# Kernel optimization log

Measured on AMD Instinct MI355X. Metric: run time of the kernel, lower is better.

The kernel has to match this reference:

```python
import jax, jax.numpy as jnp
import numpy as np

DECAY = 0.99
EPS = 1e-05


def setup_inputs() -> dict:
    key = jax.random.key(0)
    k1, k2, k3, k4 = jax.random.split(key, 4)
    B, T, D, K = 16, 4096, 128, 1024
    return {
        "z": jax.random.normal(k1, (B, T, D), dtype=jnp.float32),
        "embedding": jax.random.normal(k2, (K, D), dtype=jnp.float32),
        "cluster_size": jax.random.uniform(k3, (K,), dtype=jnp.float32),
        "ema_w": jax.random.normal(k4, (K, D), dtype=jnp.float32),
    }


def reference(z, embedding, cluster_size, ema_w):
    B, T, D = z.shape
    K = embedding.shape[0]
    z_flat = z.reshape(B * T, D)

    # Squared-distance matrix [N, K]: ||z||^2 - 2 z E^T + ||E||^2
    dist = (
        jnp.sum(z_flat * z_flat, axis=1, keepdims=True)
        - 2.0 * (z_flat @ embedding.T)
        + jnp.sum(embedding * embedding, axis=1)
    )
    indices = jnp.argmin(dist, axis=1)  # [N]
    z_q = embedding[indices].reshape(B, T, D)

    # EMA codebook update (training branch); segment_sum == one_hot.T @ z, one_hot.sum(0)
    batch_cluster = jax.ops.segment_sum(
        jnp.ones((B * T,), dtype=z.dtype), indices, num_segments=K
    )
    new_cluster_size = cluster_size * DECAY + (1.0 - DECAY) * batch_cluster
    batch_ema = jax.ops.segment_sum(z_flat, indices, num_segments=K)
    new_ema_w = ema_w * DECAY + (1.0 - DECAY) * batch_ema

    n = jnp.sum(new_cluster_size)
    smoothed = (new_cluster_size + EPS) / (n + K * EPS) * n
    new_embedding = new_ema_w / smoothed[:, None]

    # Commitment loss on OLD codebook vectors (matches torch order of ops)
    loss_vq = jnp.mean(jnp.square(jax.lax.stop_gradient(z_q) - z))
    # Straight-through estimator
    z_q_st = z + jax.lax.stop_gradient(z_q - z)

    return (
        z_q_st,
        indices.reshape(B, T),
        loss_vq,
        new_embedding,
        new_cluster_size,
        new_ema_w,
    )
```

## Files before the change

kernel.cpp:

```cpp
#include <hip/hip_runtime.h>

#define K_CODES 1024
#define D_DIM 128
#define N_ROWS 65536
#define DECAY_F 0.99f
#define OMD_F 0.01f
#define EPS_F 1e-5f

#define EPAD 144
#define CHUNK_CODES 64
#define N_CHUNKS 16
#define CHUNK_USHORT (2 * CHUNK_CODES * EPAD)
#define NT 2
#define SEG_TILE 64

#define WS_CNT     0
#define WS_LOSS    1024
#define WS_BE      1028
#define WS_ZERO_END (1028 + 131072)
#define WS_ENORM   132100
#define WS_SMOOTH  133124
#define WS_CUR     134148
#define WS_FIDX    135172
#define WS_BUCKET  200708
#define WS_SCODE   266244
#define WS_EIMG    331780

typedef __bf16 bf8_t __attribute__((ext_vector_type(8)));
typedef float  f4_t  __attribute__((ext_vector_type(4)));

__device__ inline unsigned short f2bf_bits(float f) {
    __bf16 h = (__bf16)f;
    return __builtin_bit_cast(unsigned short, h);
}
__device__ inline float bf_bits2f(unsigned short u) {
    __bf16 h = __builtin_bit_cast(__bf16, u);
    return (float)h;
}

__device__ inline void gld16(const void* g, void* l) {
    __builtin_amdgcn_global_load_lds(
        (const __attribute__((address_space(1))) void*)g,
        (__attribute__((address_space(3))) void*)l, 16, 0, 0);
}

__global__ void vq_prep(const float* __restrict__ emb, float* __restrict__ enorm,
                        unsigned short* __restrict__ eimg) {
    int t = blockIdx.x * blockDim.x + threadIdx.x;
    int code = t >> 5;
    int q = t & 31;
    float4 v = ((const float4*)(emb + (size_t)code * D_DIM))[q];
    int chunk = code >> 6, c = code & 63;
    size_t hbase = (size_t)chunk * CHUNK_USHORT + (size_t)c * EPAD + q * 4;
    size_t lbase = hbase + (size_t)CHUNK_CODES * EPAD;
    float vv[4] = {v.x, v.y, v.z, v.w};
    ushort4 hi, lo;
    unsigned short* hp = (unsigned short*)&hi;
    unsigned short* lp = (unsigned short*)&lo;
#pragma unroll
    for (int i = 0; i < 4; ++i) {
        unsigned short hb = f2bf_bits(vv[i]);
        hp[i] = hb;
        lp[i] = f2bf_bits(vv[i] - bf_bits2f(hb));
    }
    *(ushort4*)(eimg + hbase) = hi;
    *(ushort4*)(eimg + lbase) = lo;

    float s = v.x * v.x + v.y * v.y + v.z * v.z + v.w * v.w;
#pragma unroll
    for (int o = 1; o < 32; o <<= 1) s += __shfl_xor(s, o, 64);
    if (q == 0) enorm[code] = s;
}

__device__ inline void top2_update(float s, int code, float& s1, int& i1, float& s2, int& i2) {
    bool b1 = s < s1;
    bool b2 = s < s2;
    s2 = b1 ? s1 : (b2 ? s : s2);
    i2 = b1 ? i1 : (b2 ? code : i2);
    s1 = b1 ? s : s1;
    i1 = b1 ? code : i1;
}

__device__ inline void top2_merge(float& s1, int& i1, float& s2, int& i2,
                                  float t1, int j1, float t2, int j2) {
    bool bf = (t1 < s1) || (t1 == s1 && j1 < i1);
    float ns1 = bf ? t1 : s1;  int ni1 = bf ? j1 : i1;
    float ca  = bf ? s1 : t1;  int ia  = bf ? i1 : j1;
    float cb  = bf ? t2 : s2;  int ib  = bf ? j2 : i2;
    bool bs = (ca < cb) || (ca == cb && ia < ib);
    s1 = ns1; i1 = ni1;
    s2 = bs ? ca : cb; i2 = bs ? ia : ib;
}

__global__ __launch_bounds__(512) void vq_score(
    const float* __restrict__ z, const unsigned short* __restrict__ eimg,
    const float* __restrict__ enorm_g, const float* __restrict__ emb,
    float* __restrict__ out_zq, float* __restrict__ out_idx,
    int* __restrict__ cnt, unsigned int* __restrict__ fidx,
    float* __restrict__ loss_acc)
{
    __shared__ __align__(16) unsigned short lds[2][CHUNK_USHORT];
    __shared__ __align__(16) float lds_en[K_CODES];

    const int tid  = threadIdx.x;
    const int wv   = tid >> 6;
    const int lane = tid & 63;
    const int l16  = lane & 15;
    const int quad = lane >> 4;
    const int rowbase = blockIdx.x * 256 + wv * 32;

    if (tid < 256) ((float4*)lds_en)[tid] = ((const float4*)enorm_g)[tid];

    {
        const char* gs = (const char*)eimg;
        char* ls = (char*)&lds[0][0];
#pragma unroll
        for (int i = 0; i < 5; ++i) {
            int idx = wv * 5 + i;
            if (idx < 36) gld16(gs + idx * 1024 + lane * 16, ls + idx * 1024);
        }
    }

    bf8_t zh[NT][4], zl[NT][4];
#pragma unroll
    for (int nt = 0; nt < NT; ++nt) {
        int row = rowbase + nt * 16 + l16;
        const float* zr = z + (size_t)row * D_DIM;
#pragma unroll
        for (int ks = 0; ks < 4; ++ks) {
            const float4* p = (const float4*)(zr + ks * 32 + quad * 8);
            float4 a = p[0], b = p[1];
            float v[8] = {a.x, a.y, a.z, a.w, b.x, b.y, b.z, b.w};
#pragma unroll
            for (int i = 0; i < 8; ++i) {
                __bf16 hh = (__bf16)v[i];
                zh[nt][ks][i] = hh;
                zl[nt][ks][i] = (__bf16)(v[i] - (float)hh);
            }
        }
    }

    float s1[NT], s2[NT];
    int   i1[NT], i2[NT];
#pragma unroll
    for (int nt = 0; nt < NT; ++nt) { s1[nt] = 3.4e38f; s2[nt] = 3.4e38f; i1[nt] = 0; i2[nt] = 0; }

    __syncthreads();

    for (int c = 0; c < N_CHUNKS; ++c) {
        const int cur = c & 1;
        if (c + 1 < N_CHUNKS) {
            const char* gs = (const char*)(eimg + (size_t)(c + 1) * CHUNK_USHORT);
            char* ls = (char*)&lds[1 - cur][0];
#pragma unroll
            for (int i = 0; i < 5; ++i) {
                int idx = wv * 5 + i;
                if (idx < 36) gld16(gs + idx * 1024 + lane * 16, ls + idx * 1024);
            }
        }
        const unsigned short* buf = &lds[cur][0];

#pragma unroll
        for (int cg = 0; cg < 2; ++cg) {
            f4_t acc[2][NT];
#pragma unroll
            for (int ct = 0; ct < 2; ++ct)
#pragma unroll
                for (int nt = 0; nt < NT; ++nt) acc[ct][nt] = (f4_t)(0.f);

#pragma unroll
            for (int ks = 0; ks < 4; ++ks) {
                bf8_t ah[2], al[2];
#pragma unroll
                for (int ct = 0; ct < 2; ++ct) {
                    int cl = cg * 32 + ct * 16 + l16;
                    int base = cl * EPAD + ks * 32 + quad * 8;
                    ah[ct] = *(const bf8_t*)&buf[base];
                    al[ct] = *(const bf8_t*)&buf[CHUNK_CODES * EPAD + base];
                }
#pragma unroll
                for (int ct = 0; ct < 2; ++ct)
#pragma unroll
                    for (int nt = 0; nt < NT; ++nt) {
                        acc[ct][nt] = __builtin_amdgcn_mfma_f32_16x16x32_bf16(
                            ah[ct], zh[nt][ks], acc[ct][nt], 0, 0, 0);
                        acc[ct][nt] = __builtin_amdgcn_mfma_f32_16x16x32_bf16(
                            al[ct], zh[nt][ks], acc[ct][nt], 0, 0, 0);
                        acc[ct][nt] = __builtin_amdgcn_mfma_f32_16x16x32_bf16(
                            ah[ct], zl[nt][ks], acc[ct][nt], 0, 0, 0);
                    }
            }

#pragma unroll
            for (int ct = 0; ct < 2; ++ct) {
                int cb = c * 64 + cg * 32 + ct * 16 + quad * 4;
                float4 en4 = *(const float4*)&lds_en[cb];
                float env[4] = {en4.x, en4.y, en4.z, en4.w};
#pragma unroll
                for (int nt = 0; nt < NT; ++nt)
#pragma unroll
                    for (int r = 0; r < 4; ++r) {
                        float s = env[r] - 2.0f * acc[ct][nt][r];
                        top2_update(s, cb + r, s1[nt], i1[nt], s2[nt], i2[nt]);
                    }
            }
        }
        __syncthreads();
    }

#pragma unroll
    for (int off = 16; off <= 32; off <<= 1) {
#pragma unroll
        for (int nt = 0; nt < NT; ++nt) {
            float t1 = __shfl_xor(s1[nt], off, 64);
            int   j1 = __shfl_xor(i1[nt], off, 64);
            float t2 = __shfl_xor(s2[nt], off, 64);
            int   j2 = __shfl_xor(i2[nt], off, 64);
            top2_merge(s1[nt], i1[nt], s2[nt], i2[nt], t1, j1, t2, j2);
        }
    }

    float ls = 0.f;
#pragma unroll
    for (int nt = 0; nt < NT; ++nt) {
        int row = rowbase + nt * 16 + l16;
        int j1 = i1[nt], j2 = i2[nt];

        const float4* zp  = (const float4*)(z   + (size_t)row * D_DIM);
        const float4* e1p = (const float4*)(emb + (size_t)j1  * D_DIM);
        const float4* e2p = (const float4*)(emb + (size_t)j2  * D_DIM);

        float4 zv[8], a1[8], a2[8];
#pragma unroll
        for (int ks = 0; ks < 4; ++ks) {
            int o = ks * 8 + quad * 2;
            zv[ks * 2]     = zp[o];   zv[ks * 2 + 1] = zp[o + 1];
            a1[ks * 2]     = e1p[o];  a1[ks * 2 + 1] = e1p[o + 1];
            a2[ks * 2]     = e2p[o];  a2[ks * 2 + 1] = e2p[o + 1];
        }
        float p1 = 0.f, p2 = 0.f;
#pragma unroll
        for (int i = 0; i < 8; ++i) {
            p1 += zv[i].x * a1[i].x + zv[i].y * a1[i].y + zv[i].z * a1[i].z + zv[i].w * a1[i].w;
            p2 += zv[i].x * a2[i].x + zv[i].y * a2[i].y + zv[i].z * a2[i].z + zv[i].w * a2[i].w;
        }
        p1 += __shfl_xor(p1, 16, 64); p1 += __shfl_xor(p1, 32, 64);
        p2 += __shfl_xor(p2, 16, 64); p2 += __shfl_xor(p2, 32, 64);
        float sc1 = lds_en[j1] - 2.0f * p1;
        float sc2 = lds_en[j2] - 2.0f * p2;
        bool use2 = (sc2 < sc1) || (sc2 == sc1 && j2 < j1);
        int best = use2 ? j2 : j1;

        if (quad == 0) {
            out_idx[row] = (float)best;
            fidx[row] = (unsigned int)best;
            atomicAdd(cnt + best, 1);
        }

        float4* oz = (float4*)(out_zq + (size_t)row * D_DIM);
#pragma unroll
        for (int i = 0; i < 8; ++i) {
            float4 q = use2 ? a2[i] : a1[i];
            float4 zvv = zv[i];
            float4 df = {q.x - zvv.x, q.y - zvv.y, q.z - zvv.z, q.w - zvv.w};
            ls += df.x * df.x + df.y * df.y + df.z * df.z + df.w * df.w;
            float4 o = {zvv.x + df.x, zvv.y + df.y, zvv.z + df.z, zvv.w + df.w};
            oz[(i >> 1) * 8 + quad * 2 + (i & 1)] = o;
        }
    }

#pragma unroll
    for (int off = 32; off > 0; off >>= 1) ls += __shfl_down(ls, off, 64);
    if (lane == 0) atomicAdd(loss_acc, ls);
}

__global__ void vq_scan(const int* __restrict__ cnt, int* __restrict__ cursor)
{
    __shared__ int tmp[K_CODES];
    int k = threadIdx.x;
    int c = cnt[k];
    tmp[k] = c;
    __syncthreads();
    for (int off = 1; off < K_CODES; off <<= 1) {
        int t = (k >= off) ? tmp[k - off] : 0;
        __syncthreads();
        tmp[k] += t;
        __syncthreads();
    }
    cursor[k] = tmp[k] - c;
}

__global__ void vq_scatter(const unsigned int* __restrict__ fidx,
                           int* __restrict__ cursor, unsigned int* __restrict__ bucket,
                           int* __restrict__ scode)
{
    int row = blockIdx.x * blockDim.x + threadIdx.x;
    int k = (int)fidx[row];
    int slot = atomicAdd(cursor + k, 1);
    bucket[slot] = (unsigned int)row;
    scode[slot]  = k;
}

__global__ __launch_bounds__(128) void vq_segsum(
    const float* __restrict__ z, const unsigned int* __restrict__ bucket,
    const int* __restrict__ scode, float* __restrict__ be)
{
    __shared__ int sb[SEG_TILE];
    __shared__ int sc[SEG_TILE];
    const int tid = threadIdx.x;
    const int t0  = blockIdx.x * SEG_TILE;

    if (tid < SEG_TILE) sb[tid] = (int)bucket[t0 + tid];
    else if (tid < 2 * SEG_TILE) sc[tid - SEG_TILE] = scode[t0 + tid - SEG_TILE];
    __syncthreads();

    const int d = tid;
    float acc = 0.f;
    int cur = sc[0];

    for (int i = 0; i < SEG_TILE; i += 8) {
        float v[8];
#pragma unroll
        for (int j = 0; j < 8; ++j)
            v[j] = z[(size_t)sb[i + j] * D_DIM + d];
#pragma unroll
        for (int j = 0; j < 8; ++j) {
            int c = sc[i + j];
            if (c != cur) {
                atomicAdd(be + (size_t)cur * D_DIM + d, acc);
                acc = 0.f;
                cur = c;
            }
            acc += v[j];
        }
    }
    atomicAdd(be + (size_t)cur * D_DIM + d, acc);
}

__global__ void vq_finalize1(const float* __restrict__ cs, const int* __restrict__ cnt,
                             const float* __restrict__ loss_acc,
                             float* __restrict__ out_ncs, float* __restrict__ out_loss,
                             float* __restrict__ smoothed)
{
    __shared__ float red[K_CODES];
    int k = threadIdx.x;
    float ncs = cs[k] * DECAY_F + OMD_F * (float)cnt[k];
    out_ncs[k] = ncs;
    red[k] = ncs;
    __syncthreads();
    for (int s = 512; s > 0; s >>= 1) {
        if (k < s) red[k] += red[k + s];
        __syncthreads();
    }
    float n = red[0];
    smoothed[k] = (ncs + EPS_F) / (n + (float)K_CODES * EPS_F) * n;
    if (k == 0) out_loss[0] = loss_acc[0] / (float)((size_t)N_ROWS * D_DIM);
}

__global__ void vq_finalize2(const float* __restrict__ ema_w, const float* __restrict__ be,
                             const float* __restrict__ smoothed,
                             float* __restrict__ out_emb, float* __restrict__ out_ema)
{
    int i = blockIdx.x * blockDim.x + threadIdx.x;
    float e = ema_w[i] * DECAY_F + OMD_F * be[i];
    out_ema[i] = e;
    out_emb[i] = e / smoothed[i >> 7];
}

extern "C" void kernel_launch(void* const* d_in, const int* in_sizes, int n_in,
                              void* d_out, int out_size, void* d_ws, size_t ws_size,
                              hipStream_t stream) {
    const float* z   = (const float*)d_in[0];
    const float* emb = (const float*)d_in[1];
    const float* cs  = (const float*)d_in[2];
    const float* ema = (const float*)d_in[3];

    float* out    = (float*)d_out;
    float* o_zq   = out;
    float* o_idx  = o_zq + (size_t)N_ROWS * D_DIM;
    float* o_loss = o_idx + N_ROWS;
    float* o_emb  = o_loss + 1;
    float* o_ncs  = o_emb + K_CODES * D_DIM;
    float* o_ema  = o_ncs + K_CODES;

    float* ws = (float*)d_ws;
    int*            cnt      = (int*)(ws + WS_CNT);
    float*          lacc     = ws + WS_LOSS;
    float*          be       = ws + WS_BE;
    float*          enorm    = ws + WS_ENORM;
    float*          smoothed = ws + WS_SMOOTH;
    int*            cursor   = (int*)(ws + WS_CUR);
    unsigned int*   fidx     = (unsigned int*)(ws + WS_FIDX);
    unsigned int*   bucket   = (unsigned int*)(ws + WS_BUCKET);
    int*            scode    = (int*)(ws + WS_SCODE);
    unsigned short* eimg     = (unsigned short*)(ws + WS_EIMG);

    hipMemsetAsync(ws, 0, (size_t)WS_ZERO_END * sizeof(float), stream);
    vq_prep<<<128, 256, 0, stream>>>(emb, enorm, eimg);
    vq_score<<<256, 512, 0, stream>>>(z, eimg, enorm, emb,
                                      o_zq, o_idx, cnt, fidx, lacc);
    vq_scan<<<1, K_CODES, 0, stream>>>(cnt, cursor);
    vq_scatter<<<N_ROWS / 256, 256, 0, stream>>>(fidx, cursor, bucket, scode);
    vq_segsum<<<N_ROWS / SEG_TILE, 128, 0, stream>>>(z, bucket, scode, be);
    vq_finalize1<<<1, K_CODES, 0, stream>>>(cs, cnt, lacc, o_ncs, o_loss, smoothed);
    vq_finalize2<<<K_CODES * D_DIM / 256, 256, 0, stream>>>(ema, be, smoothed, o_emb, o_ema);
}
```

Before: 228.7 us.

## Deepen codebook LDS pipeline with XOR-swizzled layout and merge finalize1 into scan

```diff
diff --git a/kernel.cpp b/kernel.cpp
--- a/kernel.cpp
+++ b/kernel.cpp
@@ -7,10 +7,10 @@
 #define OMD_F 0.01f
 #define EPS_F 1e-5f
 
-#define EPAD 144
-#define CHUNK_CODES 64
-#define N_CHUNKS 16
-#define CHUNK_USHORT (2 * CHUNK_CODES * EPAD)
+#define N_HALF 16
+#define HALF_USHORT 16384
+#define HALF_BYTES 32768
+#define NSLOT 4
 #define NT 2
 #define SEG_TILE 64
 
@@ -44,15 +44,22 @@
         (__attribute__((address_space(3))) void*)l, 16, 0, 0);
 }
 
+#define SBAR() do { __builtin_amdgcn_sched_barrier(0); \
+                    __builtin_amdgcn_s_barrier(); \
+                    __builtin_amdgcn_sched_barrier(0); } while (0)
+#define SCHEDB() __builtin_amdgcn_sched_barrier(0)
+
 __global__ void vq_prep(const float* __restrict__ emb, float* __restrict__ enorm,
                         unsigned short* __restrict__ eimg) {
     int t = blockIdx.x * blockDim.x + threadIdx.x;
     int code = t >> 5;
     int q = t & 31;
     float4 v = ((const float4*)(emb + (size_t)code * D_DIM))[q];
-    int chunk = code >> 6, c = code & 63;
-    size_t hbase = (size_t)chunk * CHUNK_USHORT + (size_t)c * EPAD + q * 4;
-    size_t lbase = hbase + (size_t)CHUNK_CODES * EPAD;
+    int H = code >> 6, lc = code & 63;
+    int s  = q >> 1;
+    int sw = s ^ (lc & 7);
+    size_t hbase = (size_t)H * HALF_USHORT + lc * 128 + sw * 8 + (q & 1) * 4;
+    size_t lbase = hbase + 8192;
     float vv[4] = {v.x, v.y, v.z, v.w};
     ushort4 hi, lo;
     unsigned short* hp = (unsigned short*)&hi;
@@ -66,10 +73,10 @@
     *(ushort4*)(eimg + hbase) = hi;
     *(ushort4*)(eimg + lbase) = lo;
 
-    float s = v.x * v.x + v.y * v.y + v.z * v.z + v.w * v.w;
-#pragma unroll
-    for (int o = 1; o < 32; o <<= 1) s += __shfl_xor(s, o, 64);
-    if (q == 0) enorm[code] = s;
+    float s2 = v.x * v.x + v.y * v.y + v.z * v.z + v.w * v.w;
+#pragma unroll
+    for (int o = 1; o < 32; o <<= 1) s2 += __shfl_xor(s2, o, 64);
+    if (q == 0) enorm[code] = s2;
 }
 
 __device__ inline void top2_update(float s, int code, float& s1, int& i1, float& s2, int& i2) {
@@ -92,6 +99,76 @@
     s2 = bs ? ca : cb; i2 = bs ? ia : ib;
 }
 
+template<int WAITN, bool STAGE>
+__device__ __forceinline__ void half_body(
+    int h, const char* __restrict__ eimg_b, char* ldsx, const float* lds_en,
+    const bf8_t (&zh)[NT][4], const bf8_t (&zl)[NT][4],
+    int wv, int lane, int l16, int quad,
+    float (&s1)[NT], int (&i1)[NT], float (&s2)[NT], int (&i2)[NT])
+{
+    const unsigned short* buf = (const unsigned short*)(ldsx + (h & 3) * HALF_BYTES);
+#pragma unroll
+    for (int cg = 0; cg < 2; ++cg) {
+        bf8_t ah[2][4], al[2][4];
+#pragma unroll
+        for (int ks = 0; ks < 4; ++ks)
+#pragma unroll
+            for (int ct = 0; ct < 2; ++ct) {
+                int lc = cg * 32 + ct * 16 + l16;
+                int s  = ks * 4 + quad;
+                int off = lc * 128 + ((s ^ (lc & 7)) * 8);
+                ah[ct][ks] = *(const bf8_t*)&buf[off];
+                al[ct][ks] = *(const bf8_t*)&buf[off + 8192];
+            }
+        if (STAGE) {
+            const char* gs = eimg_b + (size_t)(h + 3) * HALF_BYTES;
+            char* ls = ldsx + ((h + 3) & 3) * HALF_BYTES;
+            int i0 = wv * 4 + cg * 2;
+            gld16(gs + (size_t)i0 * 1024 + lane * 16, ls + i0 * 1024);
+            gld16(gs + (size_t)(i0 + 1) * 1024 + lane * 16, ls + (i0 + 1) * 1024);
+            SCHEDB();
+        }
+        if (cg == 1) {
+            asm volatile("s_waitcnt vmcnt(%0)" :: "n"(WAITN) : "memory");
+        }
+        SBAR();
+        __builtin_amdgcn_s_setprio(1);
+        f4_t acc[2][NT];
+#pragma unroll
+        for (int ct = 0; ct < 2; ++ct)
+#pragma unroll
+            for (int nt = 0; nt < NT; ++nt) acc[ct][nt] = (f4_t)(0.f);
+#pragma unroll
+        for (int ks = 0; ks < 4; ++ks)
+#pragma unroll
+            for (int ct = 0; ct < 2; ++ct)
+#pragma unroll
+                for (int nt = 0; nt < NT; ++nt) {
+                    acc[ct][nt] = __builtin_amdgcn_mfma_f32_16x16x32_bf16(
+                        ah[ct][ks], zh[nt][ks], acc[ct][nt], 0, 0, 0);
+                    acc[ct][nt] = __builtin_amdgcn_mfma_f32_16x16x32_bf16(
+                        al[ct][ks], zh[nt][ks], acc[ct][nt], 0, 0, 0);
+                    acc[ct][nt] = __builtin_amdgcn_mfma_f32_16x16x32_bf16(
+                        ah[ct][ks], zl[nt][ks], acc[ct][nt], 0, 0, 0);
+                }
+        __builtin_amdgcn_s_setprio(0);
+        SBAR();
+#pragma unroll
+        for (int ct = 0; ct < 2; ++ct) {
+            int cb = h * 64 + cg * 32 + ct * 16 + quad * 4;
+            float4 en4 = *(const float4*)&lds_en[cb];
+            float env[4] = {en4.x, en4.y, en4.z, en4.w};
+#pragma unroll
+            for (int nt = 0; nt < NT; ++nt)
+#pragma unroll
+                for (int r = 0; r < 4; ++r) {
+                    float sc = env[r] - 2.0f * acc[ct][nt][r];
+                    top2_update(sc, cb + r, s1[nt], i1[nt], s2[nt], i2[nt]);
+                }
+        }
+    }
+}
+
 __global__ __launch_bounds__(512) void vq_score(
     const float* __restrict__ z, const unsigned short* __restrict__ eimg,
     const float* __restrict__ enorm_g, const float* __restrict__ emb,
@@ -99,7 +176,7 @@
     int* __restrict__ cnt, unsigned int* __restrict__ fidx,
     float* __restrict__ loss_acc)
 {
-    __shared__ __align__(16) unsigned short lds[2][CHUNK_USHORT];
+    __shared__ __align__(16) char ldsx[NSLOT * HALF_BYTES];
     __shared__ __align__(16) float lds_en[K_CODES];
 
     const int tid  = threadIdx.x;
@@ -108,18 +185,9 @@
     const int l16  = lane & 15;
     const int quad = lane >> 4;
     const int rowbase = blockIdx.x * 256 + wv * 32;
+    const char* eimg_b = (const char*)eimg;
 
     if (tid < 256) ((float4*)lds_en)[tid] = ((const float4*)enorm_g)[tid];
-
-    {
-        const char* gs = (const char*)eimg;
-        char* ls = (char*)&lds[0][0];
-#pragma unroll
-        for (int i = 0; i < 5; ++i) {
-            int idx = wv * 5 + i;
-            if (idx < 36) gld16(gs + idx * 1024 + lane * 16, ls + idx * 1024);
-        }
-    }
 
     bf8_t zh[NT][4], zl[NT][4];
 #pragma unroll
@@ -140,73 +208,35 @@
         }
     }
 
+    asm volatile("s_waitcnt vmcnt(0)" ::: "memory");
+    SCHEDB();
+
+#pragma unroll
+    for (int hh = 0; hh < 3; ++hh) {
+        const char* gs = eimg_b + (size_t)hh * HALF_BYTES;
+        char* ls = ldsx + hh * HALF_BYTES;
+#pragma unroll
+        for (int i = 0; i < 4; ++i) {
+            int idx = wv * 4 + i;
+            gld16(gs + (size_t)idx * 1024 + lane * 16, ls + idx * 1024);
+        }
+    }
+    SCHEDB();
+
     float s1[NT], s2[NT];
     int   i1[NT], i2[NT];
 #pragma unroll
     for (int nt = 0; nt < NT; ++nt) { s1[nt] = 3.4e38f; s2[nt] = 3.4e38f; i1[nt] = 0; i2[nt] = 0; }
 
-    __syncthreads();
-
-    for (int c = 0; c < N_CHUNKS; ++c) {
-        const int cur = c & 1;
-        if (c + 1 < N_CHUNKS) {
-            const char* gs = (const char*)(eimg + (size_t)(c + 1) * CHUNK_USHORT);
-            char* ls = (char*)&lds[1 - cur][0];
-#pragma unroll
-            for (int i = 0; i < 5; ++i) {
-                int idx = wv * 5 + i;
-                if (idx < 36) gld16(gs + idx * 1024 + lane * 16, ls + idx * 1024);
-            }
-        }
-        const unsigned short* buf = &lds[cur][0];
-
-#pragma unroll
-        for (int cg = 0; cg < 2; ++cg) {
-            f4_t acc[2][NT];
-#pragma unroll
-            for (int ct = 0; ct < 2; ++ct)
-#pragma unroll
-                for (int nt = 0; nt < NT; ++nt) acc[ct][nt] = (f4_t)(0.f);
-
-#pragma unroll
-            for (int ks = 0; ks < 4; ++ks) {
-                bf8_t ah[2], al[2];
-#pragma unroll
-                for (int ct = 0; ct < 2; ++ct) {
-                    int cl = cg * 32 + ct * 16 + l16;
-                    int base = cl * EPAD + ks * 32 + quad * 8;
-                    ah[ct] = *(const bf8_t*)&buf[base];
-                    al[ct] = *(const bf8_t*)&buf[CHUNK_CODES * EPAD + base];
-                }
-#pragma unroll
-                for (int ct = 0; ct < 2; ++ct)
-#pragma unroll
-                    for (int nt = 0; nt < NT; ++nt) {
-                        acc[ct][nt] = __builtin_amdgcn_mfma_f32_16x16x32_bf16(
-                            ah[ct], zh[nt][ks], acc[ct][nt], 0, 0, 0);
-                        acc[ct][nt] = __builtin_amdgcn_mfma_f32_16x16x32_bf16(
-                            al[ct], zh[nt][ks], acc[ct][nt], 0, 0, 0);
-                        acc[ct][nt] = __builtin_amdgcn_mfma_f32_16x16x32_bf16(
-                            ah[ct], zl[nt][ks], acc[ct][nt], 0, 0, 0);
-                    }
-            }
-
-#pragma unroll
-            for (int ct = 0; ct < 2; ++ct) {
-                int cb = c * 64 + cg * 32 + ct * 16 + quad * 4;
-                float4 en4 = *(const float4*)&lds_en[cb];
-                float env[4] = {en4.x, en4.y, en4.z, en4.w};
-#pragma unroll
-                for (int nt = 0; nt < NT; ++nt)
-#pragma unroll
-                    for (int r = 0; r < 4; ++r) {
-                        float s = env[r] - 2.0f * acc[ct][nt][r];
-                        top2_update(s, cb + r, s1[nt], i1[nt], s2[nt], i2[nt]);
-                    }
-            }
-        }
-        __syncthreads();
-    }
+    asm volatile("s_waitcnt vmcnt(8)" ::: "memory");
+    asm volatile("s_waitcnt lgkmcnt(0)" ::: "memory");
+    SBAR();
+
+    for (int h = 0; h < 13; ++h)
+        half_body<8, true >(h, eimg_b, ldsx, lds_en, zh, zl, wv, lane, l16, quad, s1, i1, s2, i2);
+    half_body<4, false>(13, eimg_b, ldsx, lds_en, zh, zl, wv, lane, l16, quad, s1, i1, s2, i2);
+    half_body<0, false>(14, eimg_b, ldsx, lds_en, zh, zl, wv, lane, l16, quad, s1, i1, s2, i2);
+    half_body<0, false>(15, eimg_b, ldsx, lds_en, zh, zl, wv, lane, l16, quad, s1, i1, s2, i2);
 
 #pragma unroll
     for (int off = 16; off <= 32; off <<= 1) {
@@ -274,9 +304,13 @@
     if (lane == 0) atomicAdd(loss_acc, ls);
 }
 
-__global__ void vq_scan(const int* __restrict__ cnt, int* __restrict__ cursor)
+__global__ void vq_scan(const int* __restrict__ cnt, int* __restrict__ cursor,
+                        const float* __restrict__ cs, const float* __restrict__ lacc,
+                        float* __restrict__ out_ncs, float* __restrict__ out_loss,
+                        float* __restrict__ smoothed)
 {
     __shared__ int tmp[K_CODES];
+    __shared__ float fr[16];
     int k = threadIdx.x;
     int c = cnt[k];
     tmp[k] = c;
@@ -288,6 +322,19 @@
         __syncthreads();
     }
     cursor[k] = tmp[k] - c;
+
+    float ncs = cs[k] * DECAY_F + OMD_F * (float)c;
+    out_ncs[k] = ncs;
+    float s = ncs;
+#pragma unroll
+    for (int o = 1; o < 64; o <<= 1) s += __shfl_xor(s, o, 64);
+    if ((k & 63) == 0) fr[k >> 6] = s;
+    __syncthreads();
+    float n = 0.f;
+#pragma unroll
+    for (int i = 0; i < 16; ++i) n += fr[i];
+    smoothed[k] = (ncs + EPS_F) / (n + (float)K_CODES * EPS_F) * n;
+    if (k == 0) out_loss[0] = lacc[0] / (float)((size_t)N_ROWS * D_DIM);
 }
 
 __global__ void vq_scatter(const unsigned int* __restrict__ fidx,
@@ -335,26 +382,6 @@
         }
     }
     atomicAdd(be + (size_t)cur * D_DIM + d, acc);
-}
-
-__global__ void vq_finalize1(const float* __restrict__ cs, const int* __restrict__ cnt,
-                             const float* __restrict__ loss_acc,
-                             float* __restrict__ out_ncs, float* __restrict__ out_loss,
-                             float* __restrict__ smoothed)
-{
-    __shared__ float red[K_CODES];
-    int k = threadIdx.x;
-    float ncs = cs[k] * DECAY_F + OMD_F * (float)cnt[k];
-    out_ncs[k] = ncs;
-    red[k] = ncs;
-    __syncthreads();
-    for (int s = 512; s > 0; s >>= 1) {
-        if (k < s) red[k] += red[k + s];
-        __syncthreads();
-    }
-    float n = red[0];
-    smoothed[k] = (ncs + EPS_F) / (n + (float)K_CODES * EPS_F) * n;
-    if (k == 0) out_loss[0] = loss_acc[0] / (float)((size_t)N_ROWS * D_DIM);
 }
 
 __global__ void vq_finalize2(const float* __restrict__ ema_w, const float* __restrict__ be,
@@ -399,9 +426,8 @@
     vq_prep<<<128, 256, 0, stream>>>(emb, enorm, eimg);
     vq_score<<<256, 512, 0, stream>>>(z, eimg, enorm, emb,
                                       o_zq, o_idx, cnt, fidx, lacc);
-    vq_scan<<<1, K_CODES, 0, stream>>>(cnt, cursor);
+    vq_scan<<<1, K_CODES, 0, stream>>>(cnt, cursor, cs, lacc, o_ncs, o_loss, smoothed);
     vq_scatter<<<N_ROWS / 256, 256, 0, stream>>>(fidx, cursor, bucket, scode);
     vq_segsum<<<N_ROWS / SEG_TILE, 128, 0, stream>>>(z, bucket, scode, be);
-    vq_finalize1<<<1, K_CODES, 0, stream>>>(cs, cnt, lacc, o_ncs, o_loss, smoothed);
     vq_finalize2<<<K_CODES * D_DIM / 256, 256, 0, stream>>>(ema, be, smoothed, o_emb, o_ema);
 }
```

Result: slower. 238.5 us (+4.3%).
